# Performance work log

Measured on AMD Instinct MI355X. Metric: run time of the kernel, lower is better.

## Reference

```python
import jax, jax.numpy as jnp
from jax import lax
import numpy as np

VTH = 0.2
DECAY = 0.25            # LIF membrane decay used by pcdmd slayers.LIFSpike (STBP-style)
DT = 0.001              # norse default integration step
TAU_SYN_INV = 200.0     # norse LSNNParameters defaults
TAU_MEM_INV = 100.0
TAU_ADAPT_INV = 1.0 / 700.0
BETA = 0.0              # module sets beta=0 (no threshold adaptation jumps)
ALPHA = 100.0           # SuperSpike surrogate slope (norse 'super' method)

@jax.custom_vjp
def spike_rect(v):
    # Heaviside forward, rectangular surrogate backward (STBP)
    return (v > 0).astype(v.dtype)

def _sr_fwd(v):
    return spike_rect(v), v

def _sr_bwd(v, g):
    return (g * (jnp.abs(v) < 0.5).astype(g.dtype),)

spike_rect.defvjp(_sr_fwd, _sr_bwd)

@jax.custom_vjp
def spike_super(v):
    # Heaviside forward, SuperSpike surrogate backward (norse 'super')
    return (v > 0).astype(v.dtype)

def _ss_fwd(v):
    return spike_super(v), v

def _ss_bwd(v, g):
    return (g / (ALPHA * jnp.abs(v) + 1.0) ** 2,)

spike_super.defvjp(_ss_fwd, _ss_bwd)

def lif_spike(x):
    # x: [..., T] -> spike train [..., T]
    # u_t = DECAY * u_{t-1} * (1 - o_{t-1}) + x_t ; o_t = H(u_t - VTH)
    xT = jnp.moveaxis(x, -1, 0)  # [T, ...]
    u0 = jnp.zeros(xT.shape[1:], x.dtype)
    def step(carry, xt):
        u, o = carry
        u = DECAY * u * (1.0 - o) + xt
        o = spike_rect(u - VTH)
        return (u, o), o
    _, out = lax.scan(step, (u0, u0), xT)
    return jnp.moveaxis(out, 0, -1)

def lsnn_recurrent(x, w_in, w_rec):
    # x: [T, B, H] input spikes; norse LSNNRecurrent lsnn_step with beta=0, v_th=VTH
    x_in = jnp.einsum('tbh,oh->tbo', x, w_in)  # input current, hoisted out of scan
    B, H = x.shape[1], w_in.shape[0]
    z0 = jnp.zeros((B, H), x.dtype)
    state0 = (z0, z0, z0, jnp.full((B, H), VTH, x.dtype))  # z, v, i, b (b starts at v_th)
    def step(state, xt):
        z, v, i, b = state
        i_jump = i + xt + z @ w_rec.T
        v_dec = v + DT * TAU_MEM_INV * (-v + i_jump)          # v_leak = 0
        i_dec = i_jump - DT * TAU_SYN_INV * i_jump
        b_dec = b + DT * TAU_ADAPT_INV * (VTH - b)
        z_new = spike_super(v_dec - b_dec)
        v_new = (1.0 - z_new) * v_dec                          # v_reset = 0
        b_new = b_dec + z_new * TAU_ADAPT_INV * BETA
        return (z_new, v_new, i_dec, b_new), z_new
    _, out = lax.scan(step, state0, x_in)
    return out  # [T, B, H]

def setup_inputs() -> dict:
    key = jax.random.key(0)
    ks = jax.random.split(key, 7)
    B, T = 64, 8192
    EEG_C, AUD_C, H, OUT = 64, 1, 10, 2
    x = jax.random.normal(ks[0], (B, 1, EEG_C + 2 * AUD_C, T), jnp.float32)
    s_in = 1.0 / float(np.sqrt(EEG_C))
    s_h = 1.0 / float(np.sqrt(H))
    return {
        'x': x,
        'w_front': jax.random.uniform(ks[1], (H, EEG_C), jnp.float32, -s_in, s_in),
        'b_front': jax.random.uniform(ks[2], (H,), jnp.float32, -s_in, s_in),
        'w_in': jax.random.uniform(ks[3], (H, H), jnp.float32, -s_h, s_h),
        'w_rec': jax.random.uniform(ks[4], (H, H), jnp.float32, -s_h, s_h),
        'w_cls': jax.random.uniform(ks[5], (OUT, H), jnp.float32, -s_h, s_h),
        'b_cls': jax.random.uniform(ks[6], (OUT,), jnp.float32, -s_h, s_h),
    }

def reference(x, w_front, b_front, w_in, w_rec, w_cls, b_cls):
    AUD_C = 1
    window_length = x.shape[-1]
    eeg = x[:, 0, AUD_C:-AUD_C, :]                              # [B, 64, T]
    eeg = jnp.einsum('bct,hc->bht', eeg, w_front) + b_front[None, :, None]
    eeg = lif_spike(eeg)                                        # spike_tanh in snn mode
    eeg = jnp.transpose(eeg, (2, 0, 1))                         # [T, B, H]
    z = lsnn_recurrent(eeg, w_in, w_rec)                        # [T, B, H]
    out = jnp.transpose(z, (1, 2, 0))                           # [B, H, T]
    out = jnp.einsum('bht,oh->bot', out, w_cls) + b_cls[None, :, None]
    out = lif_spike(out)                                        # spike_sigmoid in snn mode
    return jnp.sum(out, axis=2) / window_length                 # [B, 2]
```

## Files before the change

kernel.cpp:

```cpp
#include <hip/hip_runtime.h>
#include <cstdint>
#include <cstddef>

#define T_LEN 8192
#define BATCH 64
#define HID   10
#define CH    66
#define EEG   64
#define SM_STRIDE 8384
#define CHK   512
#define TS2   548

__global__ __launch_bounds__(256, 4) void k_front_lif(
    const float* __restrict__ x, const float* __restrict__ wf_g,
    const float* __restrict__ bf_g, unsigned short* __restrict__ smask,
    float* __restrict__ out) {
    __shared__ float wf[EEG][HID];
    __shared__ float bf[HID];
    __shared__ float yt[HID][TS2];
    int tid = threadIdx.x;
    for (int i = tid; i < EEG * HID; i += 256) {
        int h = i / EEG, c = i % EEG;
        wf[c][h] = wf_g[i];
    }
    if (tid < HID) bf[tid] = bf_g[tid];

    int chunk = blockIdx.x;
    int b     = blockIdx.y;
    if (chunk == 0) {
        for (int i = tid; i < 96; i += 256)
            ((unsigned*)(smask + (size_t)b * SM_STRIDE))[i] = 0u;
        if (b == 0)
            for (int i = tid; i < BATCH * 2; i += 256) out[i] = 0.f;
    }
    __syncthreads();

    int t0 = chunk * CHK;
    const float* xb = x + ((size_t)b * CH + 1) * T_LEN;
    for (int g = tid; g < 136; g += 256) {
        int t = t0 - 32 + 4 * g;
        if (t < 0) continue;
        float acc[4][HID];
#pragma unroll
        for (int j = 0; j < 4; ++j)
#pragma unroll
            for (int h = 0; h < HID; ++h) acc[j][h] = bf[h];
        const float* xp = xb + t;
#pragma unroll 4
        for (int c = 0; c < EEG; ++c) {
            float4 xv = *(const float4*)(xp + (size_t)c * T_LEN);
#pragma unroll
            for (int h = 0; h < HID; ++h) {
                float w = wf[c][h];
                acc[0][h] = fmaf(xv.x, w, acc[0][h]);
                acc[1][h] = fmaf(xv.y, w, acc[1][h]);
                acc[2][h] = fmaf(xv.z, w, acc[2][h]);
                acc[3][h] = fmaf(xv.w, w, acc[3][h]);
            }
        }
        int k = 4 * g;
#pragma unroll
        for (int h = 0; h < HID; ++h)
            *(float4*)&yt[h][k] =
                make_float4(acc[0][h], acc[1][h], acc[2][h], acc[3][h]);
    }
    __syncthreads();

    int w    = tid >> 6;
    int lane = tid & 63;
    int h    = lane & 15;
    int hh   = h < HID ? h : HID - 1;

    int kliv = 32 + 128 * w;
    int wl   = (chunk == 0 && w == 0) ? 0 : 32;
    int ks   = kliv - wl;
    int nf   = (128 + wl) >> 2;
    const float4* yrow = (const float4*)&yt[hh][0];
    int base = ks >> 2;

    unsigned short* smb = smask + (size_t)b * SM_STRIDE + 192 + t0 + 128 * w;
    float u = 0.f, o = 0.f;
    float4 A = yrow[base], B = yrow[base + 1], C = yrow[base + 2];
    for (int f = 0; f < nf; ++f) {
        int nx = f + 3; if (nx > nf - 1) nx = nf - 1;
        float4 D = yrow[base + nx];
        float vv[4] = {A.x, A.y, A.z, A.w};
        int kb = ks + 4 * f;
#pragma unroll
        for (int k2 = 0; k2 < 4; ++k2) {
            u = (o > 0.5f) ? vv[k2] : fmaf(0.25f, u, vv[k2]);
            bool sp = (u > 0.2f);
            o = sp ? 1.0f : 0.0f;
            unsigned long long bal = __ballot(sp);
            int k = kb + k2;
            if (k >= kliv && h == 0)
                smb[k - kliv] = (unsigned short)(bal & 0x3FFull);
        }
        A = B; B = C; C = D;
    }
}

__global__ __launch_bounds__(512) void k_lsnn(
    const unsigned short* __restrict__ smask,
    const float* __restrict__ w_in, const float* __restrict__ w_rec,
    const float* __restrict__ w_cls, const float* __restrict__ b_cls,
    float* __restrict__ out) {
    extern __shared__ float LDSBUF[];
    float* T = LDSBUF;
    float* D = LDSBUF + 1536;
    int tid = threadIdx.x;
    for (int i = tid; i < 1536; i += 512) {
        int hi = i / 768;
        int rem = i - hi * 768;
        int m = rem / 24, role = rem - m * 24;
        float s = 0.f;
        if (role < 22) {
            const float* wrow = (role < 10) ? (w_in + role * HID)
                              : (role < 12) ? (w_cls + (role - 10) * HID)
                                            : (w_rec + (role - 12) * HID);
#pragma unroll
            for (int j = 0; j < 5; ++j)
                if (m & (1u << j)) s += wrow[hi * 5 + j];
        }
        T[i] = s;
    }
    __syncthreads();
    for (int i = tid; i < 1024 * 22; i += 512) {
        int z = i / 22, role = i - z * 22;
        D[i] = T[(z & 31) * 24 + role] + T[768 + (z >> 5) * 24 + role];
    }
    __syncthreads();

    int lane = tid & 63;
    int q = lane >> 4;
    int r = lane & 15;
    int rr = r < 12 ? r : 11;
    int rrec = 12 + (r < HID ? r : 9);
    int shq = q * 16;
    int id = blockIdx.x * 32 + (tid >> 4);
    int b = id >> 7, chunk = id & 127;

    float bcl = (r == 10 || r == 11) ? b_cls[r - HID] : 0.f;

    const unsigned short* sm = smask + (size_t)b * SM_STRIDE + (size_t)chunk * 64;

    auto xlook = [&](const uint4& mv, float* X) {
        unsigned hw[8] = { mv.x & 0x3FFu, (mv.x >> 16) & 0x3FFu,
                           mv.y & 0x3FFu, (mv.y >> 16) & 0x3FFu,
                           mv.z & 0x3FFu, (mv.z >> 16) & 0x3FFu,
                           mv.w & 0x3FFu, (mv.w >> 16) & 0x3FFu };
#pragma unroll
        for (int u = 0; u < 8; ++u)
            X[u] = D[hw[u] * 22 + rr];
    };

    uint4 mB = *(const uint4*)(sm + 8);
    uint4 mC = *(const uint4*)(sm + 16);
    uint4 mD = *(const uint4*)(sm + 24);
    float Xc[8], Xn[8], Pc[8], Pn[8];
    { uint4 m0 = *(const uint4*)(sm); xlook(m0, Xc); }
#pragma unroll
    for (int u = 0; u < 8; ++u) { Pc[u] = 0.f; Pn[u] = 0.f; }

    float v = 0.f, cur = 0.f;
    unsigned zmask = 0;
    float uc = 0.f, oc = 0.f, accs = 0.f;

    for (int gr = 0; gr < 32; ++gr) {
        int nb = gr + 4; if (nb > 31) nb = 31;
        uint4 mE = *(const uint4*)(sm + (size_t)nb * 8);
        xlook(mB, Xn);
        unsigned zs[8];
#pragma unroll
        for (int u = 0; u < 8; ++u) {
            float rec = D[zmask * 22 + rrec];
            float ij = (cur + Xc[u]) + rec;
            float vd = v + 0.1f * (ij - v);
            cur = ij - 0.2f * ij;
            bool zb = vd > 0.2f;
            unsigned long long bal = __ballot(zb);
            v = zb ? 0.f : vd;
            zmask = (unsigned)(bal >> shq) & 0x3FFu;
            zs[u] = zmask;
        }
        if (gr >= 21) {
#pragma unroll
            for (int u = 0; u < 8; ++u)
                Pn[u] = D[zs[u] * 22 + rr];
        }
        if (gr >= 22) {
            bool in = (gr >= 25);
#pragma unroll
            for (int u = 0; u < 8; ++u) {
                float ci = Pc[u] + bcl;
                uc = (oc > 0.5f) ? ci : fmaf(0.25f, uc, ci);
                oc = (uc > 0.2f) ? 1.f : 0.f;
                if (in) accs += oc;
            }
        }
#pragma unroll
        for (int u = 0; u < 8; ++u) { Xc[u] = Xn[u]; Pc[u] = Pn[u]; }
        mB = mC; mC = mD; mD = mE;
    }
#pragma unroll
    for (int u = 0; u < 8; ++u) {
        float ci = Pc[u] + bcl;
        uc = (oc > 0.5f) ? ci : fmaf(0.25f, uc, ci);
        oc = (uc > 0.2f) ? 1.f : 0.f;
        accs += oc;
    }
    if (r == 10 || r == 11)
        atomicAdd(&out[b * 2 + (r - 10)], accs * (1.0f / 8192.0f));
}

extern "C" void kernel_launch(void* const* d_in, const int* in_sizes, int n_in,
                              void* d_out, int out_size, void* d_ws, size_t ws_size,
                              hipStream_t stream) {
    const float* x       = (const float*)d_in[0];
    const float* w_front = (const float*)d_in[1];
    const float* b_front = (const float*)d_in[2];
    const float* w_in    = (const float*)d_in[3];
    const float* w_rec   = (const float*)d_in[4];
    const float* w_cls   = (const float*)d_in[5];
    const float* b_cls   = (const float*)d_in[6];
    float* out = (float*)d_out;

    unsigned short* smask = (unsigned short*)d_ws;

    k_front_lif<<<dim3(16, BATCH), 256, 0, stream>>>(x, w_front, b_front, smask, out);
    k_lsnn<<<dim3(256), 512, (1536 + 1024 * 22) * sizeof(float), stream>>>(
        smask, w_in, w_rec, w_cls, b_cls, out);
}
```

Baseline: 266.7 us.

## Enlarge front-end LIF chunks to 2048 steps with prefetched inputs and vectorized weights

The front kernel now processes 2048 timesteps per block with 512 threads, so there are 4 blocks per batch instead of 16. Each of the 8 wavefronts runs the LIF scan over 256 steps with a 32-step warmup. Larger chunks cut the redundant 32-step halo recomputation and warmup overhead. The channel loop also gains a 4-deep register ring that prefetches input float4s, and weights are padded to 12 per channel so they can be read with vector LDS loads. In exchange, the grid is much smaller (256 blocks) and each block uses more LDS, which lowers parallelism and occupancy.

```diff
diff --git a/kernel.cpp b/kernel.cpp
--- a/kernel.cpp
+++ b/kernel.cpp
@@ -8,54 +8,61 @@
 #define CH    66
 #define EEG   64
 #define SM_STRIDE 8384
-#define CHK   512
-#define TS2   548
-
-__global__ __launch_bounds__(256, 4) void k_front_lif(
+#define TSF   2088
+
+__global__ __launch_bounds__(512) void k_front_lif(
     const float* __restrict__ x, const float* __restrict__ wf_g,
     const float* __restrict__ bf_g, unsigned short* __restrict__ smask,
     float* __restrict__ out) {
-    __shared__ float wf[EEG][HID];
-    __shared__ float bf[HID];
-    __shared__ float yt[HID][TS2];
+    __shared__ __align__(16) float yt[HID][TSF];
+    __shared__ __align__(16) float wf[EEG][12];
+    __shared__ __align__(16) float bf[16];
     int tid = threadIdx.x;
-    for (int i = tid; i < EEG * HID; i += 256) {
-        int h = i / EEG, c = i % EEG;
-        wf[c][h] = wf_g[i];
+    for (int i = tid; i < EEG * 12; i += 512) {
+        int c = i / 12, h = i - 12 * (i / 12);
+        wf[c][h] = (h < HID) ? wf_g[h * EEG + c] : 0.f;
     }
     if (tid < HID) bf[tid] = bf_g[tid];
 
-    int chunk = blockIdx.x;
-    int b     = blockIdx.y;
-    if (chunk == 0) {
-        for (int i = tid; i < 96; i += 256)
+    int bx = blockIdx.x;
+    int b  = blockIdx.y;
+    if (bx == 0) {
+        for (int i = tid; i < 96; i += 512)
             ((unsigned*)(smask + (size_t)b * SM_STRIDE))[i] = 0u;
         if (b == 0)
-            for (int i = tid; i < BATCH * 2; i += 256) out[i] = 0.f;
-    }
-    __syncthreads();
-
-    int t0 = chunk * CHK;
+            for (int i = tid; i < BATCH * 2; i += 512) out[i] = 0.f;
+    }
+    __syncthreads();
+
+    int t0 = bx * 2048;
     const float* xb = x + ((size_t)b * CH + 1) * T_LEN;
-    for (int g = tid; g < 136; g += 256) {
+    for (int g = tid; g < 520; g += 512) {
         int t = t0 - 32 + 4 * g;
         if (t < 0) continue;
+        const float* xp = xb + t;
+        float4 ring[4];
+#pragma unroll
+        for (int j = 0; j < 4; ++j) ring[j] = *(const float4*)(xp + (size_t)j * T_LEN);
         float acc[4][HID];
 #pragma unroll
         for (int j = 0; j < 4; ++j)
 #pragma unroll
             for (int h = 0; h < HID; ++h) acc[j][h] = bf[h];
-        const float* xp = xb + t;
 #pragma unroll 4
         for (int c = 0; c < EEG; ++c) {
-            float4 xv = *(const float4*)(xp + (size_t)c * T_LEN);
+            float4 xv = ring[c & 3];
+            if (c + 4 < EEG)
+                ring[c & 3] = *(const float4*)(xp + (size_t)(c + 4) * T_LEN);
+            float4 w0 = *(const float4*)&wf[c][0];
+            float4 w1 = *(const float4*)&wf[c][4];
+            float2 w2 = *(const float2*)&wf[c][8];
+            float w[HID] = {w0.x, w0.y, w0.z, w0.w, w1.x, w1.y, w1.z, w1.w, w2.x, w2.y};
 #pragma unroll
             for (int h = 0; h < HID; ++h) {
-                float w = wf[c][h];
-                acc[0][h] = fmaf(xv.x, w, acc[0][h]);
-                acc[1][h] = fmaf(xv.y, w, acc[1][h]);
-                acc[2][h] = fmaf(xv.z, w, acc[2][h]);
-                acc[3][h] = fmaf(xv.w, w, acc[3][h]);
+                acc[0][h] = fmaf(xv.x, w[h], acc[0][h]);
+                acc[1][h] = fmaf(xv.y, w[h], acc[1][h]);
+                acc[2][h] = fmaf(xv.z, w[h], acc[2][h]);
+                acc[3][h] = fmaf(xv.w, w[h], acc[3][h]);
             }
         }
         int k = 4 * g;
@@ -66,24 +73,24 @@
     }
     __syncthreads();
 
-    int w    = tid >> 6;
+    int s    = tid >> 6;
     int lane = tid & 63;
     int h    = lane & 15;
     int hh   = h < HID ? h : HID - 1;
 
-    int kliv = 32 + 128 * w;
-    int wl   = (chunk == 0 && w == 0) ? 0 : 32;
+    int kliv = 32 + 256 * s;
+    int wl   = (bx == 0 && s == 0) ? 0 : 32;
     int ks   = kliv - wl;
-    int nf   = (128 + wl) >> 2;
+    int nf   = (256 + wl) >> 2;
     const float4* yrow = (const float4*)&yt[hh][0];
     int base = ks >> 2;
 
-    unsigned short* smb = smask + (size_t)b * SM_STRIDE + 192 + t0 + 128 * w;
+    unsigned short* smb = smask + (size_t)b * SM_STRIDE + 192 + t0 + 256 * s;
     float u = 0.f, o = 0.f;
     float4 A = yrow[base], B = yrow[base + 1], C = yrow[base + 2];
     for (int f = 0; f < nf; ++f) {
         int nx = f + 3; if (nx > nf - 1) nx = nf - 1;
-        float4 D = yrow[base + nx];
+        float4 Dv = yrow[base + nx];
         float vv[4] = {A.x, A.y, A.z, A.w};
         int kb = ks + 4 * f;
 #pragma unroll
@@ -96,7 +103,7 @@
             if (k >= kliv && h == 0)
                 smb[k - kliv] = (unsigned short)(bal & 0x3FFull);
         }
-        A = B; B = C; C = D;
+        A = B; B = C; C = Dv;
     }
 }
 
@@ -227,7 +234,7 @@
 
     unsigned short* smask = (unsigned short*)d_ws;
 
-    k_front_lif<<<dim3(16, BATCH), 256, 0, stream>>>(x, w_front, b_front, smask, out);
+    k_front_lif<<<dim3(4, BATCH), 512, 0, stream>>>(x, w_front, b_front, smask, out);
     k_lsnn<<<dim3(256), 512, (1536 + 1024 * 22) * sizeof(float), stream>>>(
         smask, w_in, w_rec, w_cls, b_cls, out);
 }
```

After: 290.6 us. 1.09x slower.
